# Performance work log

Hardware: AMD Instinct MI355X
Metric: run time of the kernel (lower is better)

Reference implementation:

```python
import jax, jax.numpy as jnp
import numpy as np

DIM = 1024
HEADS = 16
DIM_HEAD = 64
DEPTH = 12
LN_EPS = 1e-5


def setup_inputs() -> dict:
    key = jax.random.key(0)
    k1, k2, k3 = jax.random.split(key, 3)
    B, N = 4, 2048
    inner = HEADS * DIM_HEAD
    x = jax.random.normal(k1, (B, N, DIM), dtype=jnp.float32)
    ln_w = jnp.ones((DIM,), jnp.float32)
    ln_b = jnp.zeros((DIM,), jnp.float32)
    w_qkv = jax.random.normal(k2, (DIM, 3 * inner), jnp.float32) * (DIM ** -0.5)
    w_out = jax.random.normal(k3, (inner, DIM), jnp.float32) * (inner ** -0.5)
    b_out = jnp.zeros((DIM,), jnp.float32)
    return {"x": x, "ln_w": ln_w, "ln_b": ln_b, "w_qkv": w_qkv,
            "w_out": w_out, "b_out": b_out, "layer_index": 2}


def reference(x, ln_w, ln_b, w_qkv, w_out, b_out, layer_index):
    B, N, D = x.shape
    scale = DIM_HEAD ** -0.5
    # LayerNorm
    mu = jnp.mean(x, axis=-1, keepdims=True)
    var = jnp.mean(jnp.square(x - mu), axis=-1, keepdims=True)
    xn = (x - mu) * jax.lax.rsqrt(var + LN_EPS) * ln_w + ln_b
    # QKV projection (no bias), split heads: b n (h d) -> b h n d
    qkv = xn @ w_qkv  # [B, N, 3*H*Dh]
    q, k, v = jnp.split(qkv, 3, axis=-1)
    def heads(t):
        return t.reshape(B, N, HEADS, DIM_HEAD).transpose(0, 2, 1, 3)
    q, k, v = heads(q), heads(k), heads(v)
    dots = jnp.einsum('bhnd,bhmd->bhnm', q, k) * scale  # [B,H,N,N]
    if layer_index < DEPTH // 2:
        attn = jax.nn.relu(dots)
    else:
        attn = jax.nn.softmax(dots, axis=-1)
    attn = attn / N  # divide by x.shape[1]
    out = jnp.einsum('bhnm,bhmd->bhnd', attn, v)
    out = out.transpose(0, 2, 1, 3).reshape(B, N, HEADS * DIM_HEAD)
    # to_out (heads > 1): Linear + (inactive) dropout
    return out @ w_out + b_out
```

## Files before the change

kernel.cpp:

```cpp
#include <hip/hip_runtime.h>
#include <stdint.h>

typedef __bf16 bf16x8 __attribute__((ext_vector_type(8)));
typedef __bf16 bf16x4 __attribute__((ext_vector_type(4)));
typedef float f32x4 __attribute__((ext_vector_type(4)));

#define PSCALE (0.125f / 2048.0f)

#define GLOAD16(src, dst)                                                      \
  __builtin_amdgcn_global_load_lds(                                            \
      (__attribute__((address_space(1))) void*)const_cast<__bf16*>(src),       \
      (__attribute__((address_space(3))) void*)(dst), 16, 0, 0)

__global__ __launch_bounds__(256) void prep(
    const float* __restrict__ x, const float* __restrict__ lw,
    const float* __restrict__ lb, __bf16* __restrict__ xn,
    const float* __restrict__ w_qkv, __bf16* __restrict__ Wt1,
    const float* __restrict__ w_out, __bf16* __restrict__ Wt2) {
  __shared__ __bf16 T[64][72];
  __shared__ float red[8];
  const int b = blockIdx.x;
  const int t = threadIdx.x;
  if (b < 8192) {
    const float4 v = ((const float4*)(x + (size_t)b * 1024))[t];
    float s = v.x + v.y + v.z + v.w;
    float ss = v.x * v.x + v.y * v.y + v.z * v.z + v.w * v.w;
#pragma unroll
    for (int o = 32; o; o >>= 1) {
      s += __shfl_down(s, o);
      ss += __shfl_down(ss, o);
    }
    if ((t & 63) == 0) {
      red[t >> 6] = s;
      red[4 + (t >> 6)] = ss;
    }
    __syncthreads();
    const float tot = red[0] + red[1] + red[2] + red[3];
    const float tot2 = red[4] + red[5] + red[6] + red[7];
    const float mu = tot * (1.0f / 1024.0f);
    const float var = tot2 * (1.0f / 1024.0f) - mu * mu;
    const float rs = rsqrtf(var + 1e-5f);
    const float4 wv = ((const float4*)lw)[t];
    const float4 bv = ((const float4*)lb)[t];
    bf16x4 o;
    o[0] = (__bf16)((v.x - mu) * rs * wv.x + bv.x);
    o[1] = (__bf16)((v.y - mu) * rs * wv.y + bv.y);
    o[2] = (__bf16)((v.z - mu) * rs * wv.z + bv.z);
    o[3] = (__bf16)((v.w - mu) * rs * wv.w + bv.w);
    ((bf16x4*)xn)[(size_t)b * 256 + t] = o;
    return;
  }
  const float* A;
  __bf16* At;
  int R, C, bx, by;
  if (b < 8960) {
    const int ti = b - 8192;
    A = w_qkv; At = Wt1; R = 1024; C = 3072;
    bx = ti % 48; by = ti / 48;
  } else {
    const int ti = b - 8960;
    A = w_out; At = Wt2; R = 1024; C = 1024;
    bx = ti % 16; by = ti / 16;
  }
  const int rb = by * 64, cb = bx * 64;
  const int r = t >> 2, cg = t & 3;
#pragma unroll
  for (int k = 0; k < 4; ++k) {
    const float4 v =
        *(const float4*)(A + (size_t)(rb + r) * C + cb + cg * 16 + k * 4);
    T[cg * 16 + k * 4 + 0][r] = (__bf16)v.x;
    T[cg * 16 + k * 4 + 1][r] = (__bf16)v.y;
    T[cg * 16 + k * 4 + 2][r] = (__bf16)v.z;
    T[cg * 16 + k * 4 + 3][r] = (__bf16)v.w;
  }
  __syncthreads();
#pragma unroll
  for (int i = 0; i < 2; ++i) {
    const int j = i * 256 + t;
    const int c = j >> 3, s8 = j & 7;
    const bf16x8 o = *(const bf16x8*)&T[c][s8 * 8];
    *(bf16x8*)(At + (size_t)(cb + c) * R + rb + s8 * 8) = o;
  }
}

template <int MODE>
__global__ __launch_bounds__(512) void gemm_nt(
    const __bf16* __restrict__ A, const __bf16* __restrict__ B, int K,
    float* __restrict__ outF, __bf16* __restrict__ Qo, __bf16* __restrict__ Ko,
    __bf16* __restrict__ Vto, const float* __restrict__ bias) {
  __shared__ __bf16 Sm[3 * 24576];
  const int tid = threadIdx.x;
  const int lane = tid & 63, w = tid >> 6;
  const int g = lane >> 4, c15 = lane & 15;
  const int wr = w >> 2, wc = w & 3;
  const int linear = blockIdx.y * gridDim.x + blockIdx.x;
  const int per = (gridDim.x * gridDim.y) >> 3;
  const int nl = (linear & 7) * per + (linear >> 3);
  const int rb = (nl / gridDim.x) * 128, cb = (nl % gridDim.x) * 256;

  const __bf16* aSp[2];
  const __bf16* bSp[4];
  int aDo[2], bDo[4];
#pragma unroll
  for (int i = 0; i < 2; ++i) {
    const int j = i * 512 + tid, row = j >> 3, slot = j & 7;
    aSp[i] = A + (size_t)(rb + row) * K + ((slot ^ (row & 7)) << 3);
    aDo[i] = i * 4096 + w * 512;
  }
#pragma unroll
  for (int i = 0; i < 4; ++i) {
    const int j = i * 512 + tid, col = j >> 3, slot = j & 7;
    bSp[i] = B + (size_t)(cb + col) * K + ((slot ^ (col & 7)) << 3);
    bDo[i] = 8192 + i * 4096 + w * 512;
  }

  f32x4 acc[4][4] = {};
  const int nkb = K >> 6;

#pragma unroll
  for (int t = 0; t < 2; ++t) {
    __bf16* dst = Sm + t * 24576;
#pragma unroll
    for (int i = 0; i < 2; ++i) GLOAD16(aSp[i] + t * 64, dst + aDo[i]);
#pragma unroll
    for (int i = 0; i < 4; ++i) GLOAD16(bSp[i] + t * 64, dst + bDo[i]);
  }

  int cur = 0, stg = 2, koff = 128;
  for (int kb = 0; kb < nkb; ++kb) {
    if (kb == nkb - 1) {
      asm volatile("s_waitcnt vmcnt(0)" ::: "memory");
    } else {
      asm volatile("s_waitcnt vmcnt(6)" ::: "memory");
    }
    __builtin_amdgcn_s_barrier();
    const bool do_stage = (kb < nkb - 2);
    __bf16* sdst = Sm + stg * 24576;
    if (do_stage) {
#pragma unroll
      for (int i = 0; i < 2; ++i) GLOAD16(aSp[i] + koff, sdst + aDo[i]);
    }
    const __bf16* __restrict__ Ac = Sm + cur * 24576;
    const __bf16* __restrict__ Bc = Ac + 8192;
    {
      bf16x8 af[4], bfr[4];
      const int kc = g;
#pragma unroll
      for (int rt = 0; rt < 4; ++rt) {
        const int lr = wr * 64 + rt * 16 + c15;
        af[rt] = *(const bf16x8*)(Ac + lr * 64 + ((kc ^ (lr & 7)) << 3));
      }
#pragma unroll
      for (int ct = 0; ct < 4; ++ct) {
        const int lc = wc * 64 + ct * 16 + c15;
        bfr[ct] = *(const bf16x8*)(Bc + lc * 64 + ((kc ^ (lc & 7)) << 3));
      }
      __builtin_amdgcn_s_setprio(1);
#pragma unroll
      for (int rt = 0; rt < 4; ++rt)
#pragma unroll
        for (int ct = 0; ct < 4; ++ct)
          acc[rt][ct] = __builtin_amdgcn_mfma_f32_16x16x32_bf16(
              af[rt], bfr[ct], acc[rt][ct], 0, 0, 0);
      __builtin_amdgcn_s_setprio(0);
    }
    if (do_stage) {
#pragma unroll
      for (int i = 0; i < 4; ++i) GLOAD16(bSp[i] + koff, sdst + bDo[i]);
      koff += 64;
    }
    {
      bf16x8 af[4], bfr[4];
      const int kc = 4 + g;
#pragma unroll
      for (int rt = 0; rt < 4; ++rt) {
        const int lr = wr * 64 + rt * 16 + c15;
        af[rt] = *(const bf16x8*)(Ac + lr * 64 + ((kc ^ (lr & 7)) << 3));
      }
#pragma unroll
      for (int ct = 0; ct < 4; ++ct) {
        const int lc = wc * 64 + ct * 16 + c15;
        bfr[ct] = *(const bf16x8*)(Bc + lc * 64 + ((kc ^ (lc & 7)) << 3));
      }
      __builtin_amdgcn_s_setprio(1);
#pragma unroll
      for (int rt = 0; rt < 4; ++rt)
#pragma unroll
        for (int ct = 0; ct < 4; ++ct)
          acc[rt][ct] = __builtin_amdgcn_mfma_f32_16x16x32_bf16(
              af[rt], bfr[ct], acc[rt][ct], 0, 0, 0);
      __builtin_amdgcn_s_setprio(0);
    }
    cur = (cur == 2) ? 0 : cur + 1;
    stg = (stg == 2) ? 0 : stg + 1;
  }
  const int r00 = rb + wr * 64 + g * 4;
  if (MODE == 1) {
#pragma unroll
    for (int ct = 0; ct < 4; ++ct) {
      const int col = cb + wc * 64 + ct * 16 + c15;
      const float bv = bias[col];
#pragma unroll
      for (int rt = 0; rt < 4; ++rt) {
        const int row = r00 + rt * 16;
#pragma unroll
        for (int r = 0; r < 4; ++r)
          outF[(size_t)(row + r) * 1024 + col] = acc[rt][ct][r] + bv;
      }
    }
  } else {
#pragma unroll
    for (int ct = 0; ct < 4; ++ct) {
      const int col = cb + wc * 64 + ct * 16 + c15;
      const int part = col >> 10, rem = col & 1023;
      const int h = rem >> 6, d = rem & 63;
#pragma unroll
      for (int rt = 0; rt < 4; ++rt) {
        const int row = r00 + rt * 16;
        const int bi = row >> 11, n = row & 2047;
        const size_t bh = (size_t)bi * 16 + h;
        if (part == 2) {
          bf16x4 pv;
#pragma unroll
          for (int r = 0; r < 4; ++r) pv[r] = (__bf16)acc[rt][ct][r];
          *(bf16x4*)(Vto + (bh * 64 + d) * 2048 + n) = pv;
        } else if (part == 0) {
          __bf16* dst = Qo + (bh * 2048 + n) * 64 + d;
#pragma unroll
          for (int r = 0; r < 4; ++r)
            dst[(size_t)r * 64] = (__bf16)(acc[rt][ct][r] * PSCALE);
        } else {
          __bf16* dst = Ko + (bh * 2048 + n) * 64 + d;
#pragma unroll
          for (int r = 0; r < 4; ++r) dst[(size_t)r * 64] = (__bf16)acc[rt][ct][r];
        }
      }
    }
  }
}

__global__ __launch_bounds__(512) void attn_relu(
    const __bf16* __restrict__ Q, const __bf16* __restrict__ K,
    const __bf16* __restrict__ Vt, __bf16* __restrict__ O) {
  __shared__ __bf16 Ks[2][128 * 64];
  __shared__ __bf16 Vs[2][64 * 128];
  const int tid = threadIdx.x;
  const int lane = tid & 63, w = tid >> 6;
  const int g = lane >> 4, c15 = lane & 15;
  const int bh = blockIdx.x, qb = blockIdx.y;
  const __bf16* Qg = Q + ((size_t)bh * 2048 + qb * 256) * 64;
  const __bf16* Kg = K + (size_t)bh * 2048 * 64;
  const __bf16* Vg = Vt + (size_t)bh * 64 * 2048;

  const __bf16* kp0;
  const __bf16* kp1;
  const __bf16* vp0;
  const __bf16* vp1;
  {
    const int j0 = tid, j1 = 512 + tid;
    const int r0_ = j0 >> 3, s0_ = j0 & 7;
    const int r1_ = j1 >> 3, s1_ = j1 & 7;
    const int sr0 = (r0_ & 96) | ((r0_ & 12) << 1) | ((r0_ & 16) >> 2) | (r0_ & 3);
    const int sr1 = (r1_ & 96) | ((r1_ & 12) << 1) | ((r1_ & 16) >> 2) | (r1_ & 3);
    kp0 = Kg + (size_t)sr0 * 64 + ((s0_ ^ (r0_ & 7)) << 3);
    kp1 = Kg + (size_t)sr1 * 64 + ((s1_ ^ (r1_ & 7)) << 3);
    const int d0_ = j0 >> 4, t0_ = j0 & 15;
    const int d1_ = j1 >> 4, t1_ = j1 & 15;
    vp0 = Vg + (size_t)d0_ * 2048 + ((t0_ ^ (d0_ & 15)) << 3);
    vp1 = Vg + (size_t)d1_ * 2048 + ((t1_ ^ (d1_ & 15)) << 3);
  }
  const int dstoff = w * 64 * 8;

  bf16x8 qf[2][2];
#pragma unroll
  for (int rt = 0; rt < 2; ++rt)
#pragma unroll
    for (int ks = 0; ks < 2; ++ks) {
      const int row = w * 32 + rt * 16 + c15;
      qf[rt][ks] = *(const bf16x8*)(Qg + row * 64 + ks * 32 + (g << 3));
    }
  f32x4 oacc[2][4] = {};

  GLOAD16(kp0, Ks[0] + dstoff);
  GLOAD16(kp1, Ks[0] + 512 * 8 + dstoff);
  GLOAD16(vp0, Vs[0] + dstoff);
  GLOAD16(vp1, Vs[0] + 512 * 8 + dstoff);
  kp0 += 128 * 64; kp1 += 128 * 64; vp0 += 128; vp1 += 128;

  for (int kb = 0; kb < 16; ++kb) {
    const int cur = kb & 1;
    if (kb < 15) {
      GLOAD16(kp0, Ks[cur ^ 1] + dstoff);
      GLOAD16(kp1, Ks[cur ^ 1] + 512 * 8 + dstoff);
      GLOAD16(vp0, Vs[cur ^ 1] + dstoff);
      GLOAD16(vp1, Vs[cur ^ 1] + 512 * 8 + dstoff);
      kp0 += 128 * 64; kp1 += 128 * 64; vp0 += 128; vp1 += 128;
      asm volatile("s_waitcnt vmcnt(4)" ::: "memory");
    } else {
      asm volatile("s_waitcnt vmcnt(0)" ::: "memory");
    }
    __builtin_amdgcn_s_barrier();
    const __bf16* __restrict__ Kc = Ks[cur];
    const __bf16* __restrict__ Vc = Vs[cur];
#pragma unroll
    for (int u = 0; u < 4; ++u) {
      const int kra = u * 32 + c15;
      const int krb = u * 32 + 16 + c15;
      const bf16x8 kfa0 = *(const bf16x8*)(Kc + kra * 64 + ((g ^ (kra & 7)) << 3));
      const bf16x8 kfa1 = *(const bf16x8*)(Kc + kra * 64 + (((4 + g) ^ (kra & 7)) << 3));
      const bf16x8 kfb0 = *(const bf16x8*)(Kc + krb * 64 + ((g ^ (krb & 7)) << 3));
      const bf16x8 kfb1 = *(const bf16x8*)(Kc + krb * 64 + (((4 + g) ^ (krb & 7)) << 3));
      f32x4 sa[2] = {{}, {}}, sb[2] = {{}, {}};
      __builtin_amdgcn_s_setprio(1);
#pragma unroll
      for (int rt = 0; rt < 2; ++rt) {
        sa[rt] = __builtin_amdgcn_mfma_f32_16x16x32_bf16(kfa0, qf[rt][0], sa[rt], 0, 0, 0);
        sa[rt] = __builtin_amdgcn_mfma_f32_16x16x32_bf16(kfa1, qf[rt][1], sa[rt], 0, 0, 0);
        sb[rt] = __builtin_amdgcn_mfma_f32_16x16x32_bf16(kfb0, qf[rt][0], sb[rt], 0, 0, 0);
        sb[rt] = __builtin_amdgcn_mfma_f32_16x16x32_bf16(kfb1, qf[rt][1], sb[rt], 0, 0, 0);
      }
      __builtin_amdgcn_s_setprio(0);
      bf16x8 pa[2];
#pragma unroll
      for (int rt = 0; rt < 2; ++rt)
#pragma unroll
        for (int r = 0; r < 4; ++r) {
          pa[rt][r] = (__bf16)fmaxf(sa[rt][r], 0.0f);
          pa[rt][4 + r] = (__bf16)fmaxf(sb[rt][r], 0.0f);
        }
      __builtin_amdgcn_s_setprio(1);
#pragma unroll
      for (int dt = 0; dt < 4; ++dt) {
        const int d = dt * 16 + c15;
        const bf16x8 vb = *(const bf16x8*)(Vc + d * 128 + (((4 * u + g) ^ c15) << 3));
#pragma unroll
        for (int rt = 0; rt < 2; ++rt)
          oacc[rt][dt] = __builtin_amdgcn_mfma_f32_16x16x32_bf16(
              pa[rt], vb, oacc[rt][dt], 0, 0, 0);
      }
      __builtin_amdgcn_s_setprio(0);
    }
    __builtin_amdgcn_s_barrier();
  }
  const int bi = bh >> 4, h = bh & 15;
#pragma unroll
  for (int rt = 0; rt < 2; ++rt)
#pragma unroll
    for (int dt = 0; dt < 4; ++dt) {
      const int col = h * 64 + dt * 16 + c15;
      const int n0 = qb * 256 + w * 32 + rt * 16 + g * 4;
      __bf16* dst = O + ((size_t)bi * 2048 + n0) * 1024 + col;
#pragma unroll
      for (int r = 0; r < 4; ++r) dst[(size_t)r * 1024] = (__bf16)oacc[rt][dt][r];
    }
}

extern "C" void kernel_launch(void* const* d_in, const int* in_sizes, int n_in,
                              void* d_out, int out_size, void* d_ws,
                              size_t ws_size, hipStream_t stream) {
  (void)in_sizes; (void)n_in; (void)out_size; (void)ws_size;
  const float* x = (const float*)d_in[0];
  const float* ln_w = (const float*)d_in[1];
  const float* ln_b = (const float*)d_in[2];
  const float* w_qkv = (const float*)d_in[3];
  const float* w_out = (const float*)d_in[4];
  const float* b_out = (const float*)d_in[5];
  char* ws = (char*)d_ws;
  __bf16* xn = (__bf16*)(ws);
  __bf16* Wt1 = (__bf16*)(ws + (size_t)(16u << 20));
  __bf16* Wt2 = (__bf16*)(ws + (size_t)(22u << 20));
  __bf16* Qb = (__bf16*)(ws + (size_t)(24u << 20));
  __bf16* Kb = (__bf16*)(ws + (size_t)(40u << 20));
  __bf16* Vtb = (__bf16*)(ws + (size_t)(56u << 20));
  __bf16* Ob = (__bf16*)(ws + (size_t)(72u << 20));
  float* out = (float*)d_out;

  prep<<<9216, 256, 0, stream>>>(x, ln_w, ln_b, xn, w_qkv, Wt1, w_out, Wt2);
  gemm_nt<0><<<dim3(12, 64), 512, 0, stream>>>(xn, Wt1, 1024, nullptr, Qb, Kb,
                                               Vtb, nullptr);
  attn_relu<<<dim3(64, 8), 512, 0, stream>>>(Qb, Kb, Vtb, Ob);
  gemm_nt<1><<<dim3(4, 64), 512, 0, stream>>>(Ob, Wt2, 1024, out, nullptr,
                                              nullptr, nullptr, b_out);
}
```

Baseline: 159.4 us.

## Switch ReLU attention kernel to 32x32x16 MFMA tiles

Rewrites the ReLU attention inner loop to use 32x32x16 bf16 MFMA instructions in place of 16x16x32. The K-tile row permutation, the Q fragment loads, the V fragment indexing and the output store mapping all change to fit the 32-lane layout. Larger MFMA tiles cut the instruction count and the LDS fragment reloads per FLOP. In exchange the accumulators become 16-wide vectors, which raises register pressure. It also adds a min-blocks hint of 4 to launch_bounds.

```diff
diff --git a/kernel.cpp b/kernel.cpp
--- a/kernel.cpp
+++ b/kernel.cpp
@@ -4,6 +4,7 @@
 typedef __bf16 bf16x8 __attribute__((ext_vector_type(8)));
 typedef __bf16 bf16x4 __attribute__((ext_vector_type(4)));
 typedef float f32x4 __attribute__((ext_vector_type(4)));
+typedef float f32x16 __attribute__((ext_vector_type(16)));
 
 #define PSCALE (0.125f / 2048.0f)
 
@@ -239,14 +240,14 @@
   }
 }
 
-__global__ __launch_bounds__(512) void attn_relu(
+__global__ __launch_bounds__(512, 4) void attn_relu(
     const __bf16* __restrict__ Q, const __bf16* __restrict__ K,
     const __bf16* __restrict__ Vt, __bf16* __restrict__ O) {
   __shared__ __bf16 Ks[2][128 * 64];
   __shared__ __bf16 Vs[2][64 * 128];
   const int tid = threadIdx.x;
-  const int lane = tid & 63, w = tid >> 6;
-  const int g = lane >> 4, c15 = lane & 15;
+  const int lane = tid & 63, wv = tid >> 6;
+  const int hi = lane >> 5, c31 = lane & 31;
   const int bh = blockIdx.x, qb = blockIdx.y;
   const __bf16* Qg = Q + ((size_t)bh * 2048 + qb * 256) * 64;
   const __bf16* Kg = K + (size_t)bh * 2048 * 64;
@@ -258,28 +259,24 @@
   const __bf16* vp1;
   {
     const int j0 = tid, j1 = 512 + tid;
-    const int r0_ = j0 >> 3, s0_ = j0 & 7;
-    const int r1_ = j1 >> 3, s1_ = j1 & 7;
-    const int sr0 = (r0_ & 96) | ((r0_ & 12) << 1) | ((r0_ & 16) >> 2) | (r0_ & 3);
-    const int sr1 = (r1_ & 96) | ((r1_ & 12) << 1) | ((r1_ & 16) >> 2) | (r1_ & 3);
-    kp0 = Kg + (size_t)sr0 * 64 + ((s0_ ^ (r0_ & 7)) << 3);
-    kp1 = Kg + (size_t)sr1 * 64 + ((s1_ ^ (r1_ & 7)) << 3);
+    const int X0 = j0 >> 3, s0 = j0 & 7;
+    const int X1 = j1 >> 3, s1 = j1 & 7;
+    const int K0 = (X0 & ~12) | ((X0 & 4) << 1) | ((X0 & 8) >> 1);
+    const int K1 = (X1 & ~12) | ((X1 & 4) << 1) | ((X1 & 8) >> 1);
+    kp0 = Kg + (size_t)K0 * 64 + ((s0 ^ (X0 & 7)) << 3);
+    kp1 = Kg + (size_t)K1 * 64 + ((s1 ^ (X1 & 7)) << 3);
     const int d0_ = j0 >> 4, t0_ = j0 & 15;
     const int d1_ = j1 >> 4, t1_ = j1 & 15;
     vp0 = Vg + (size_t)d0_ * 2048 + ((t0_ ^ (d0_ & 15)) << 3);
     vp1 = Vg + (size_t)d1_ * 2048 + ((t1_ ^ (d1_ & 15)) << 3);
   }
-  const int dstoff = w * 64 * 8;
-
-  bf16x8 qf[2][2];
-#pragma unroll
-  for (int rt = 0; rt < 2; ++rt)
-#pragma unroll
-    for (int ks = 0; ks < 2; ++ks) {
-      const int row = w * 32 + rt * 16 + c15;
-      qf[rt][ks] = *(const bf16x8*)(Qg + row * 64 + ks * 32 + (g << 3));
-    }
-  f32x4 oacc[2][4] = {};
+  const int dstoff = wv * 64 * 8;
+
+  bf16x8 qf[4];
+#pragma unroll
+  for (int dw = 0; dw < 4; ++dw)
+    qf[dw] = *(const bf16x8*)(Qg + (wv * 32 + c31) * 64 + dw * 16 + hi * 8);
+  f32x16 oacc[2] = {};
 
   GLOAD16(kp0, Ks[0] + dstoff);
   GLOAD16(kp1, Ks[0] + 512 * 8 + dstoff);
@@ -303,40 +300,37 @@
     const __bf16* __restrict__ Kc = Ks[cur];
     const __bf16* __restrict__ Vc = Vs[cur];
 #pragma unroll
-    for (int u = 0; u < 4; ++u) {
-      const int kra = u * 32 + c15;
-      const int krb = u * 32 + 16 + c15;
-      const bf16x8 kfa0 = *(const bf16x8*)(Kc + kra * 64 + ((g ^ (kra & 7)) << 3));
-      const bf16x8 kfa1 = *(const bf16x8*)(Kc + kra * 64 + (((4 + g) ^ (kra & 7)) << 3));
-      const bf16x8 kfb0 = *(const bf16x8*)(Kc + krb * 64 + ((g ^ (krb & 7)) << 3));
-      const bf16x8 kfb1 = *(const bf16x8*)(Kc + krb * 64 + (((4 + g) ^ (krb & 7)) << 3));
-      f32x4 sa[2] = {{}, {}}, sb[2] = {{}, {}};
+    for (int kb32 = 0; kb32 < 4; ++kb32) {
+      bf16x8 kf[4];
+      const int R = kb32 * 32 + c31;
+#pragma unroll
+      for (int dw = 0; dw < 4; ++dw)
+        kf[dw] =
+            *(const bf16x8*)(Kc + R * 64 + (((2 * dw + hi) ^ (R & 7)) << 3));
+      f32x16 s = {};
       __builtin_amdgcn_s_setprio(1);
 #pragma unroll
-      for (int rt = 0; rt < 2; ++rt) {
-        sa[rt] = __builtin_amdgcn_mfma_f32_16x16x32_bf16(kfa0, qf[rt][0], sa[rt], 0, 0, 0);
-        sa[rt] = __builtin_amdgcn_mfma_f32_16x16x32_bf16(kfa1, qf[rt][1], sa[rt], 0, 0, 0);
-        sb[rt] = __builtin_amdgcn_mfma_f32_16x16x32_bf16(kfb0, qf[rt][0], sb[rt], 0, 0, 0);
-        sb[rt] = __builtin_amdgcn_mfma_f32_16x16x32_bf16(kfb1, qf[rt][1], sb[rt], 0, 0, 0);
-      }
+      for (int dw = 0; dw < 4; ++dw)
+        s = __builtin_amdgcn_mfma_f32_32x32x16_bf16(kf[dw], qf[dw], s, 0, 0, 0);
       __builtin_amdgcn_s_setprio(0);
       bf16x8 pa[2];
 #pragma unroll
-      for (int rt = 0; rt < 2; ++rt)
-#pragma unroll
-        for (int r = 0; r < 4; ++r) {
-          pa[rt][r] = (__bf16)fmaxf(sa[rt][r], 0.0f);
-          pa[rt][4 + r] = (__bf16)fmaxf(sb[rt][r], 0.0f);
+      for (int wl = 0; wl < 2; ++wl)
+#pragma unroll
+        for (int e = 0; e < 8; ++e)
+          pa[wl][e] = (__bf16)fmaxf(s[8 * wl + e], 0.0f);
+      __builtin_amdgcn_s_setprio(1);
+#pragma unroll
+      for (int wl = 0; wl < 2; ++wl) {
+        const int win = 2 * kb32 + wl;
+#pragma unroll
+        for (int dc = 0; dc < 2; ++dc) {
+          const int d = dc * 32 + c31;
+          const bf16x8 vb = *(const bf16x8*)(
+              Vc + d * 128 + (((2 * win + hi) ^ (d & 15)) << 3));
+          oacc[dc] = __builtin_amdgcn_mfma_f32_32x32x16_bf16(pa[wl], vb,
+                                                             oacc[dc], 0, 0, 0);
         }
-      __builtin_amdgcn_s_setprio(1);
-#pragma unroll
-      for (int dt = 0; dt < 4; ++dt) {
-        const int d = dt * 16 + c15;
-        const bf16x8 vb = *(const bf16x8*)(Vc + d * 128 + (((4 * u + g) ^ c15) << 3));
-#pragma unroll
-        for (int rt = 0; rt < 2; ++rt)
-          oacc[rt][dt] = __builtin_amdgcn_mfma_f32_16x16x32_bf16(
-              pa[rt], vb, oacc[rt][dt], 0, 0, 0);
       }
       __builtin_amdgcn_s_setprio(0);
     }
@@ -344,15 +338,15 @@
   }
   const int bi = bh >> 4, h = bh & 15;
 #pragma unroll
-  for (int rt = 0; rt < 2; ++rt)
-#pragma unroll
-    for (int dt = 0; dt < 4; ++dt) {
-      const int col = h * 64 + dt * 16 + c15;
-      const int n0 = qb * 256 + w * 32 + rt * 16 + g * 4;
-      __bf16* dst = O + ((size_t)bi * 2048 + n0) * 1024 + col;
-#pragma unroll
-      for (int r = 0; r < 4; ++r) dst[(size_t)r * 1024] = (__bf16)oacc[rt][dt][r];
-    }
+  for (int dc = 0; dc < 2; ++dc) {
+    const int col = h * 64 + dc * 32 + c31;
+#pragma unroll
+    for (int r = 0; r < 16; ++r) {
+      const int q = wv * 32 + (r & 3) + 8 * (r >> 2) + 4 * hi;
+      const int n0 = qb * 256 + q;
+      O[((size_t)bi * 2048 + n0) * 1024 + col] = (__bf16)oacc[dc][r];
+    }
+  }
 }
 
 extern "C" void kernel_launch(void* const* d_in, const int* in_sizes, int n_in,
```

After: 161.0 us. About the same (+1.0%).
